# Kernel tuning notes

Hardware: AMD Instinct MI355X
Metric: run time of the kernel (lower is better)

Reference implementation:

```python
import jax, jax.numpy as jnp
import numpy as np

NUM_HEADS = 8
EPS = 1e-6


def conv1x1(x, w, b):
    # x: [b,c,h,w], w: [out,in], b: [out]  (torch Conv2d 1x1 weight squeezed)
    return jnp.einsum('bchw,oc->bohw', x, w) + b[None, :, None, None]


def feature_map(x):
    return jax.nn.elu(x) + 1.0


def setup_inputs() -> dict:
    key = jax.random.key(0)
    ks = jax.random.split(key, 9)
    C = 512
    s = 1.0 / np.sqrt(C)
    x = jax.random.normal(ks[0], (8, C, 64, 64), dtype=jnp.float32)
    wq = jax.random.normal(ks[1], (C, C), dtype=jnp.float32) * s
    wk = jax.random.normal(ks[2], (C, C), dtype=jnp.float32) * s
    wv = jax.random.normal(ks[3], (C, C), dtype=jnp.float32) * s
    wo = jax.random.normal(ks[4], (C, C), dtype=jnp.float32) * s
    bq = jax.random.normal(ks[5], (C,), dtype=jnp.float32) * 0.01
    bk = jax.random.normal(ks[6], (C,), dtype=jnp.float32) * 0.01
    bv = jax.random.normal(ks[7], (C,), dtype=jnp.float32) * 0.01
    bo = jax.random.normal(ks[8], (C,), dtype=jnp.float32) * 0.01
    return {'x': x, 'wq': wq, 'bq': bq, 'wk': wk, 'bk': bk,
            'wv': wv, 'bv': bv, 'wo': wo, 'bo': bo}


def reference(x, wq, bq, wk, bk, wv, bv, wo, bo):
    b, c, h, w = x.shape
    nh = NUM_HEADS
    hd = c // nh
    L = h * w

    def to_heads(t):
        # [b,c,h,w] -> [b,nh,L,hd]
        return t.reshape(b, nh, hd, L).transpose(0, 1, 3, 2)

    Q = feature_map(to_heads(conv1x1(x, wq, bq)))
    K = feature_map(to_heads(conv1x1(x, wk, bk)))
    V = to_heads(conv1x1(x, wv, bv)) / L  # values / v_length

    KV = jnp.einsum('bhld,bhlv->bhdv', K, V)                 # [b,nh,hd,hd]
    Z = 1.0 / (jnp.einsum('bhld,bhd->bhl', Q, K.sum(axis=-2)) + EPS)
    out = jnp.einsum('bhld,bhdv,bhl->bhlv', Q, KV, Z) * L    # [b,nh,L,hd]

    out = out.transpose(0, 1, 3, 2).reshape(b, c, h, w)
    return conv1x1(out, wo, bo)
```

## Files before the change

kernel.cpp:

```cpp
#include <hip/hip_runtime.h>
#include <hip/hip_bf16.h>
#include <stdint.h>

#define BATCH 8
#define CCH   512
#define NHD   8
#define HD    64
#define LLEN  4096
#define M1    1536

typedef __bf16 bf16x8 __attribute__((ext_vector_type(8)));
typedef __bf16 bf16x4 __attribute__((ext_vector_type(4)));
typedef float  f32x4  __attribute__((ext_vector_type(4)));

__device__ __forceinline__ f32x4 mfma16(bf16x8 a, bf16x8 b, f32x4 c) {
  return __builtin_amdgcn_mfma_f32_16x16x32_bf16(a, b, c, 0, 0, 0);
}

__device__ __forceinline__ void gload_lds16(const void* g, void* l) {
  __builtin_amdgcn_global_load_lds(
      (const __attribute__((address_space(1))) uint32_t*)(uintptr_t)g,
      (__attribute__((address_space(3))) uint32_t*)(uintptr_t)l,
      16, 0, 0);
}

__global__ void pack_w(const float* __restrict__ wq, const float* __restrict__ wk,
                       const float* __restrict__ wv, const float* __restrict__ wo,
                       const float* __restrict__ bq, const float* __restrict__ bk,
                       const float* __restrict__ bv,
                       __bf16* __restrict__ wqkvb, __bf16* __restrict__ wob,
                       float* __restrict__ biasq) {
  const int n = M1 * CCH + CCH * CCH + M1;
  for (int i = blockIdx.x * blockDim.x + threadIdx.x; i < n; i += gridDim.x * blockDim.x) {
    if (i < M1 * CCH) {
      int r = i >> 9, c = i & 511;
      float v = (r < 512) ? wq[r * 512 + c]
              : (r < 1024) ? wk[(r - 512) * 512 + c]
                           : wv[(r - 1024) * 512 + c];
      wqkvb[i] = (__bf16)v;
    } else if (i < M1 * CCH + CCH * CCH) {
      int j = i - M1 * CCH;
      wob[j] = (__bf16)wo[j];
    } else {
      int j = i - M1 * CCH - CCH * CCH;
      biasq[j] = (j < 512) ? bq[j] : (j < 1024) ? bk[j - 512] : bv[j - 1024];
    }
  }
}

__global__ __launch_bounds__(256) void transpose_x(const float* __restrict__ x,
                                                   __bf16* __restrict__ xt) {
  __shared__ float tile[64][65];
  const int b = blockIdx.z, c0 = blockIdx.y * 64, l0 = blockIdx.x * 64;
  const int t = threadIdx.x;
  const int lq = (t & 15) * 4, cr = t >> 4;
  const float* xp = x + ((size_t)b * CCH + c0) * LLEN + l0;
#pragma unroll
  for (int q = 0; q < 4; ++q) {
    const int c = cr + q * 16;
    float4 v = *(const float4*)(xp + (size_t)c * LLEN + lq);
    tile[c][lq + 0] = v.x;
    tile[c][lq + 1] = v.y;
    tile[c][lq + 2] = v.z;
    tile[c][lq + 3] = v.w;
  }
  __syncthreads();
  __bf16* xo = xt + ((size_t)b * LLEN + l0) * CCH + c0;
  const int c4 = (t & 15) * 4, lr = t >> 4;
#pragma unroll
  for (int p = 0; p < 4; ++p) {
    const int l = lr + p * 16;
    bf16x4 o;
#pragma unroll
    for (int i = 0; i < 4; ++i) o[i] = (__bf16)tile[c4 + i][l];
    *(bf16x4*)(xo + (size_t)l * CCH + c4) = o;
  }
}

#define STAGE4(tt)                                                           \
  {                                                                          \
    const int tK = (tt) * 32;                                                \
    const int bs = ((tt) % 3) * 16384;                                       \
    gload_lds16(Ag + sOff + tK,         lds + bs + tid * 8);                 \
    gload_lds16(Ag + sOff + 65536 + tK, lds + bs + 4096 + tid * 8);          \
    gload_lds16(Bg + sOff + tK,         lds + bs + 8192 + tid * 8);          \
    gload_lds16(Bg + sOff + 65536 + tK, lds + bs + 12288 + tid * 8);         \
  }
#define READS12(tt)                                                          \
  {                                                                          \
    const int rb = ((tt) % 3) * 16384;                                       \
    const int s = (tt) & 1;                                                  \
    _Pragma("unroll") for (int m = 0; m < 8; ++m)                            \
        aS[s][m] = *(const bf16x8*)(lds + rb + aLane + m * 512);             \
    _Pragma("unroll") for (int n = 0; n < 4; ++n)                            \
        bS[s][n] = *(const bf16x8*)(lds + rb + bLane + n * 512);             \
  }

template <int EPI>
__global__ __launch_bounds__(512, 2) void gemm256(
    const __bf16* __restrict__ A, const __bf16* __restrict__ Bm,
    const float* __restrict__ bias,
    __bf16* __restrict__ qt, __bf16* __restrict__ kcm, __bf16* __restrict__ vcm,
    float* __restrict__ out) {
  __shared__ __attribute__((aligned(16))) __bf16 lds[3 * 16384];
  const int b  = blockIdx.z;
  const int n0 = blockIdx.x * 256;
  const int m0 = blockIdx.y * 256;
  const int tid = threadIdx.x;
  const int ll = tid & 63, w = tid >> 6;
  const int wr = w >> 2, wc = w & 3;
  const int lhi = ll >> 4, llo = ll & 15;

  const int Ra = wr * 128 + llo;
  const int aLane = ((Ra >> 1) << 6) + (((((Ra & 1) << 2) | lhi) ^ ((Ra >> 1) & 7)) << 3);
  const int Rb = wc * 64 + llo;
  const int bLane = 8192 + ((Rb >> 1) << 6) + (((((Rb & 1) << 2) | lhi) ^ ((Rb >> 1) & 7)) << 3);

  const int r2s = tid >> 3, c7u = (tid & 7) ^ (r2s & 7);
  const int sRow = (r2s << 1) | (c7u >> 2);
  const int sOff = sRow * CCH + ((c7u & 3) << 3);

  const __bf16* Ag = A + (size_t)m0 * CCH;
  const __bf16* Bg = Bm + ((size_t)b * LLEN + n0) * CCH;

  bf16x8 aS[2][8], bS[2][4];
  f32x4 acc[8][4] = {};

  STAGE4(0)
  STAGE4(1)
  asm volatile("s_waitcnt vmcnt(4)" ::: "memory");
  asm volatile("s_barrier" ::: "memory");
  READS12(0)

#pragma unroll
  for (int t = 0; t < 16; ++t) {
    asm volatile("s_barrier" ::: "memory");
    if (t < 14) STAGE4(t + 2)
    if (t < 14) asm volatile("s_waitcnt vmcnt(4)" ::: "memory");
    else        asm volatile("s_waitcnt vmcnt(0)" ::: "memory");
    asm volatile("s_barrier" ::: "memory");
    if (t < 15) READS12(t + 1)
    if (t < 15) asm volatile("s_waitcnt lgkmcnt(12)" ::: "memory");
    else        asm volatile("s_waitcnt lgkmcnt(0)" ::: "memory");
    __builtin_amdgcn_sched_barrier(0);
    __builtin_amdgcn_s_setprio(1);
    {
      const int s = t & 1;
#pragma unroll
      for (int m = 0; m < 8; ++m)
#pragma unroll
        for (int n = 0; n < 4; ++n) acc[m][n] = mfma16(aS[s][m], bS[s][n], acc[m][n]);
    }
    __builtin_amdgcn_s_setprio(0);
  }

#pragma unroll
  for (int i = 0; i < 8; ++i) {
    const int o0 = m0 + wr * 128 + i * 16 + lhi * 4;
#pragma unroll
    for (int j = 0; j < 4; ++j) {
      const int col = n0 + wc * 64 + j * 16 + llo;
      if (EPI == 0) {
        if (m0 < 512) {
          bf16x4 pk;
#pragma unroll
          for (int r = 0; r < 4; ++r) {
            float tv = acc[i][j][r] + bias[o0 + r];
            tv = tv > 0.f ? tv + 1.f : __expf(tv);
            pk[r] = (__bf16)tv;
          }
          *(bf16x4*)(qt + ((size_t)b * LLEN + col) * CCH + o0) = pk;
        } else if (m0 < 1024) {
#pragma unroll
          for (int r = 0; r < 4; ++r) {
            float tv = acc[i][j][r] + bias[o0 + r];
            tv = tv > 0.f ? tv + 1.f : __expf(tv);
            kcm[((size_t)b * CCH + (o0 - 512 + r)) * LLEN + col] = (__bf16)tv;
          }
        } else {
#pragma unroll
          for (int r = 0; r < 4; ++r)
            vcm[((size_t)b * CCH + (o0 - 1024 + r)) * LLEN + col] =
                (__bf16)(acc[i][j][r] + bias[o0 + r]);
        }
      } else {
#pragma unroll
        for (int r = 0; r < 4; ++r)
          out[((size_t)b * CCH + o0 + r) * LLEN + col] = acc[i][j][r] + bias[o0 + r];
      }
    }
  }
}

__global__ __launch_bounds__(256) void kv_part_k(const __bf16* __restrict__ kcm,
                                                 const __bf16* __restrict__ vcm,
                                                 float* __restrict__ part,
                                                 float* __restrict__ part_ks) {
  __shared__ float red[8192];
  __shared__ float ksred[4][64];
  const int lc = blockIdx.x, bh = blockIdx.y;
  const int b = bh >> 3, h = bh & 7;
  const int tid = threadIdx.x;
  const int w = tid >> 6, ll = tid & 63, lhi = ll >> 4, llo = ll & 15;
  const __bf16* Kp = kcm + ((size_t)b * CCH + h * 64) * LLEN;
  const __bf16* Vp = vcm + ((size_t)b * CCH + h * 64) * LLEN;
  f32x4 acc[4][4];
#pragma unroll
  for (int i = 0; i < 4; ++i)
#pragma unroll
    for (int j = 0; j < 4; ++j) acc[i][j] = (f32x4){0.f, 0.f, 0.f, 0.f};
  float ks[4] = {0.f, 0.f, 0.f, 0.f};
  const int base = lc * 512 + w * 128 + lhi * 8;
#pragma unroll
  for (int kt = 0; kt < 4; ++kt) {
    const int k0 = base + kt * 32;
    bf16x8 af[4], bfr[4];
#pragma unroll
    for (int i = 0; i < 4; ++i) af[i]  = *(const bf16x8*)(Kp + (size_t)(i * 16 + llo) * LLEN + k0);
#pragma unroll
    for (int i = 0; i < 4; ++i) bfr[i] = *(const bf16x8*)(Vp + (size_t)(i * 16 + llo) * LLEN + k0);
#pragma unroll
    for (int i = 0; i < 4; ++i)
#pragma unroll
      for (int r = 0; r < 8; ++r) ks[i] += (float)af[i][r];
#pragma unroll
    for (int i = 0; i < 4; ++i)
#pragma unroll
      for (int j = 0; j < 4; ++j) acc[i][j] = mfma16(af[i], bfr[j], acc[i][j]);
  }
#pragma unroll
  for (int i = 0; i < 4; ++i) {
    float s = ks[i];
    s += __shfl_xor(s, 16);
    s += __shfl_xor(s, 32);
    if (lhi == 0) ksred[w][i * 16 + llo] = s;
  }
  if (w >= 2) {
#pragma unroll
    for (int i = 0; i < 4; ++i)
#pragma unroll
      for (int j = 0; j < 4; ++j)
        *(f32x4*)(red + (((w - 2) * 16 + i * 4 + j) << 8) + ll * 4) = acc[i][j];
  }
  __syncthreads();
  if (w < 2) {
#pragma unroll
    for (int i = 0; i < 4; ++i)
#pragma unroll
      for (int j = 0; j < 4; ++j)
        acc[i][j] += *(const f32x4*)(red + ((w * 16 + i * 4 + j) << 8) + ll * 4);
  }
  float ksv = 0.f;
  if (w == 1) ksv = ksred[0][ll] + ksred[1][ll] + ksred[2][ll] + ksred[3][ll];
  __syncthreads();
  if (w == 1) {
#pragma unroll
    for (int i = 0; i < 4; ++i)
#pragma unroll
      for (int j = 0; j < 4; ++j)
        *(f32x4*)(red + ((i * 4 + j) << 8) + ll * 4) = acc[i][j];
    part_ks[((size_t)lc * 64 + bh) * 64 + ll] = ksv;
  }
  __syncthreads();
  if (w == 0) {
    float* op = part + ((size_t)lc * 64 + bh) * 4096;
#pragma unroll
    for (int i = 0; i < 4; ++i)
#pragma unroll
      for (int j = 0; j < 4; ++j) {
        acc[i][j] += *(const f32x4*)(red + ((i * 4 + j) << 8) + ll * 4);
#pragma unroll
        for (int r = 0; r < 4; ++r) {
          int d = i * 16 + lhi * 4 + r, v = j * 16 + llo;
          op[d * 64 + v] = acc[i][j][r];
        }
      }
  }
}

__global__ void kv_red_k(const float* __restrict__ part, float* __restrict__ kv) {
  const int i = blockIdx.x * blockDim.x + threadIdx.x;
  float s = 0.f;
#pragma unroll
  for (int lc = 0; lc < 8; ++lc) s += part[(size_t)lc * 262144 + i];
  kv[i] = s;
}

__global__ void ksum_red_k(const float* __restrict__ part_ks, float* __restrict__ ksum) {
  const int i = blockIdx.x * blockDim.x + threadIdx.x;
  float s = 0.f;
#pragma unroll
  for (int lc = 0; lc < 8; ++lc) s += part_ks[(size_t)lc * 4096 + i];
  ksum[i] = s;
}

__global__ __launch_bounds__(256) void apply_k(const __bf16* __restrict__ qt,
                                               const float* __restrict__ kv,
                                               const float* __restrict__ ksum,
                                               __bf16* __restrict__ attn) {
  __shared__ __attribute__((aligned(16))) __bf16 kvT[64 * 68];
  __shared__ float zb[256];
  const int lc = blockIdx.x, bh = blockIdx.y;
  const int b = bh >> 3, h = bh & 7;
  const int tid = threadIdx.x;
  const float* kvp = kv + (size_t)bh * 4096;
  for (int i = tid; i < 4096; i += 256) {
    int d = i >> 6, v = i & 63;
    kvT[v * 68 + d] = (__bf16)kvp[i];
  }
  const int l = lc * 256 + tid;
  const __bf16* qp = qt + ((size_t)b * LLEN + l) * CCH + h * 64;
  const float* ksp = ksum + bh * 64;
  float s = 0.f;
#pragma unroll
  for (int d8 = 0; d8 < 64; d8 += 8) {
    bf16x8 qv = *(const bf16x8*)(qp + d8);
#pragma unroll
    for (int i = 0; i < 8; ++i) s += (float)qv[i] * ksp[d8 + i];
  }
  zb[tid] = 1.0f / (s + 1e-6f);
  __syncthreads();

  const int ll = tid & 63, w = tid >> 6, lhi = ll >> 4, llo = ll & 15;
  f32x4 acc[4][4];
#pragma unroll
  for (int i = 0; i < 4; ++i)
#pragma unroll
    for (int j = 0; j < 4; ++j) acc[i][j] = (f32x4){0.f, 0.f, 0.f, 0.f};
  const __bf16* qbase = qt + ((size_t)b * LLEN + lc * 256 + w * 64) * CCH + h * 64;
#pragma unroll
  for (int kt = 0; kt < 2; ++kt) {
    const int k8 = kt * 32 + lhi * 8;
    bf16x8 af[4], bfr[4];
#pragma unroll
    for (int i = 0; i < 4; ++i)
      af[i] = *(const bf16x8*)(qbase + (size_t)(i * 16 + llo) * CCH + k8);
#pragma unroll
    for (int j = 0; j < 4; ++j) {
      const __bf16* pb = kvT + (j * 16 + llo) * 68 + k8;
      ((bf16x4*)&bfr[j])[0] = *(const bf16x4*)pb;
      ((bf16x4*)&bfr[j])[1] = *(const bf16x4*)(pb + 4);
    }
#pragma unroll
    for (int i = 0; i < 4; ++i)
#pragma unroll
      for (int j = 0; j < 4; ++j) acc[i][j] = mfma16(af[i], bfr[j], acc[i][j]);
  }
  __bf16* ap = attn + ((size_t)b * LLEN + lc * 256) * CCH + h * 64;
#pragma unroll
  for (int i = 0; i < 4; ++i)
#pragma unroll
    for (int j = 0; j < 4; ++j)
#pragma unroll
      for (int r = 0; r < 4; ++r) {
        int ml = w * 64 + i * 16 + lhi * 4 + r;
        int v = j * 16 + llo;
        ap[(size_t)ml * CCH + v] = (__bf16)(acc[i][j][r] * zb[ml]);
      }
}

extern "C" void kernel_launch(void* const* d_in, const int* in_sizes, int n_in,
                              void* d_out, int out_size, void* d_ws, size_t ws_size,
                              hipStream_t stream) {
  const float* x  = (const float*)d_in[0];
  const float* wq = (const float*)d_in[1];
  const float* bq = (const float*)d_in[2];
  const float* wk = (const float*)d_in[3];
  const float* bk = (const float*)d_in[4];
  const float* wv = (const float*)d_in[5];
  const float* bv = (const float*)d_in[6];
  const float* wo = (const float*)d_in[7];
  const float* bo = (const float*)d_in[8];
  float* out = (float*)d_out;

  char* p = (char*)d_ws;
  __bf16* xt    = (__bf16*)p; p += (size_t)BATCH * LLEN * CCH * 2;
  __bf16* qt    = (__bf16*)p; p += (size_t)BATCH * LLEN * CCH * 2;
  __bf16* kcm   = (__bf16*)p; p += (size_t)BATCH * CCH * LLEN * 2;
  __bf16* vcm   = (__bf16*)p; p += (size_t)BATCH * CCH * LLEN * 2;
  __bf16* wqkvb = (__bf16*)p; p += (size_t)M1 * CCH * 2;
  __bf16* wob   = (__bf16*)p; p += (size_t)CCH * CCH * 2;
  float*  biasq = (float*)p;  p += (size_t)M1 * 4;
  float*  ksum  = (float*)p;  p += (size_t)BATCH * CCH * 4;
  float*  part  = (float*)p;  p += (size_t)8 * 64 * HD * HD * 4;
  float*  kvb   = (float*)p;  p += (size_t)64 * HD * HD * 4;
  float*  pks   = (float*)p;  p += (size_t)8 * 64 * 64 * 4;
  __bf16* attn  = xt;

  pack_w<<<1024, 256, 0, stream>>>(wq, wk, wv, wo, bq, bk, bv, wqkvb, wob, biasq);
  transpose_x<<<dim3(64, 8, BATCH), 256, 0, stream>>>(x, xt);
  gemm256<0><<<dim3(16, 6, BATCH), 512, 0, stream>>>(wqkvb, xt, biasq, qt, kcm, vcm, nullptr);
  kv_part_k<<<dim3(8, 64), 256, 0, stream>>>(kcm, vcm, part, pks);
  kv_red_k<<<1024, 256, 0, stream>>>(part, kvb);
  ksum_red_k<<<16, 256, 0, stream>>>(pks, ksum);
  apply_k<<<dim3(16, 64), 256, 0, stream>>>(qt, kvb, ksum, attn);
  gemm256<1><<<dim3(16, 2, BATCH), 512, 0, stream>>>(wob, attn, bo, nullptr, nullptr, nullptr, out);
}
```

Baseline: 170.2 us.

## Restructure GEMM main loop into split-phase ping-pong with 4-stage LDS ring

Replaces the 3-buffer LDS ring and register double-buffered fragments with a 4-buffer ring. Each K step is now split into two half-MFMA phases that interleave LDS fragment reads and the A/B global->LDS prefetch halves, separated by barriers. Launch bounds drop to 1 block per CU to allow the larger LDS footprint and more registers. The intent is to overlap memory and compute the way ping-pong schedules do, at the cost of more barriers per iteration, lower occupancy, and a loop that is no longer forced to unroll.

```diff
diff --git a/kernel.cpp b/kernel.cpp
--- a/kernel.cpp
+++ b/kernel.cpp
@@ -77,32 +77,28 @@
   }
 }
 
-#define STAGE4(tt)                                                           \
+#define STAGE_A2(tt)                                                         \
   {                                                                          \
+    const int bs = ((tt) & 3) * 16384;                                       \
     const int tK = (tt) * 32;                                                \
-    const int bs = ((tt) % 3) * 16384;                                       \
     gload_lds16(Ag + sOff + tK,         lds + bs + tid * 8);                 \
     gload_lds16(Ag + sOff + 65536 + tK, lds + bs + 4096 + tid * 8);          \
+  }
+#define STAGE_B2(tt)                                                         \
+  {                                                                          \
+    const int bs = ((tt) & 3) * 16384;                                       \
+    const int tK = (tt) * 32;                                                \
     gload_lds16(Bg + sOff + tK,         lds + bs + 8192 + tid * 8);          \
     gload_lds16(Bg + sOff + 65536 + tK, lds + bs + 12288 + tid * 8);         \
   }
-#define READS12(tt)                                                          \
-  {                                                                          \
-    const int rb = ((tt) % 3) * 16384;                                       \
-    const int s = (tt) & 1;                                                  \
-    _Pragma("unroll") for (int m = 0; m < 8; ++m)                            \
-        aS[s][m] = *(const bf16x8*)(lds + rb + aLane + m * 512);             \
-    _Pragma("unroll") for (int n = 0; n < 4; ++n)                            \
-        bS[s][n] = *(const bf16x8*)(lds + rb + bLane + n * 512);             \
-  }
 
 template <int EPI>
-__global__ __launch_bounds__(512, 2) void gemm256(
+__global__ __launch_bounds__(512, 1) void gemm256(
     const __bf16* __restrict__ A, const __bf16* __restrict__ Bm,
     const float* __restrict__ bias,
     __bf16* __restrict__ qt, __bf16* __restrict__ kcm, __bf16* __restrict__ vcm,
     float* __restrict__ out) {
-  __shared__ __attribute__((aligned(16))) __bf16 lds[3 * 16384];
+  __shared__ __attribute__((aligned(16))) __bf16 lds[4 * 16384];
   const int b  = blockIdx.z;
   const int n0 = blockIdx.x * 256;
   const int m0 = blockIdx.y * 256;
@@ -123,35 +119,46 @@
   const __bf16* Ag = A + (size_t)m0 * CCH;
   const __bf16* Bg = Bm + ((size_t)b * LLEN + n0) * CCH;
 
-  bf16x8 aS[2][8], bS[2][4];
   f32x4 acc[8][4] = {};
 
-  STAGE4(0)
-  STAGE4(1)
+  STAGE_A2(0) STAGE_B2(0)
+  STAGE_A2(1) STAGE_B2(1)
   asm volatile("s_waitcnt vmcnt(4)" ::: "memory");
   asm volatile("s_barrier" ::: "memory");
-  READS12(0)
-
-#pragma unroll
+
   for (int t = 0; t < 16; ++t) {
+    const int cb = (t & 3) * 16384;
+    bf16x8 af[4], bfr[4];
+#pragma unroll
+    for (int m = 0; m < 4; ++m) af[m] = *(const bf16x8*)(lds + cb + aLane + m * 512);
+#pragma unroll
+    for (int n = 0; n < 4; ++n) bfr[n] = *(const bf16x8*)(lds + cb + bLane + n * 512);
+    if (t <= 13) STAGE_A2(t + 2)
     asm volatile("s_barrier" ::: "memory");
-    if (t < 14) STAGE4(t + 2)
-    if (t < 14) asm volatile("s_waitcnt vmcnt(4)" ::: "memory");
-    else        asm volatile("s_waitcnt vmcnt(0)" ::: "memory");
-    asm volatile("s_barrier" ::: "memory");
-    if (t < 15) READS12(t + 1)
-    if (t < 15) asm volatile("s_waitcnt lgkmcnt(12)" ::: "memory");
-    else        asm volatile("s_waitcnt lgkmcnt(0)" ::: "memory");
+    asm volatile("s_waitcnt lgkmcnt(0)" ::: "memory");
     __builtin_amdgcn_sched_barrier(0);
     __builtin_amdgcn_s_setprio(1);
-    {
-      const int s = t & 1;
-#pragma unroll
-      for (int m = 0; m < 8; ++m)
-#pragma unroll
-        for (int n = 0; n < 4; ++n) acc[m][n] = mfma16(aS[s][m], bS[s][n], acc[m][n]);
-    }
+#pragma unroll
+    for (int m = 0; m < 4; ++m)
+#pragma unroll
+      for (int n = 0; n < 4; ++n) acc[m][n] = mfma16(af[m], bfr[n], acc[m][n]);
     __builtin_amdgcn_s_setprio(0);
+    asm volatile("s_barrier" ::: "memory");
+#pragma unroll
+    for (int m = 0; m < 4; ++m) af[m] = *(const bf16x8*)(lds + cb + aLane + (m + 4) * 512);
+    if (t <= 13) STAGE_B2(t + 2)
+    asm volatile("s_barrier" ::: "memory");
+    asm volatile("s_waitcnt lgkmcnt(0)" ::: "memory");
+    __builtin_amdgcn_sched_barrier(0);
+    __builtin_amdgcn_s_setprio(1);
+#pragma unroll
+    for (int m = 0; m < 4; ++m)
+#pragma unroll
+      for (int n = 0; n < 4; ++n) acc[m + 4][n] = mfma16(af[m], bfr[n], acc[m + 4][n]);
+    __builtin_amdgcn_s_setprio(0);
+    if (t < 14)       asm volatile("s_waitcnt vmcnt(4)" ::: "memory");
+    else if (t == 14) asm volatile("s_waitcnt vmcnt(0)" ::: "memory");
+    asm volatile("s_barrier" ::: "memory");
   }
 
 #pragma unroll
```

New measurement: 176.1 us. +3.4%, slower.

## Pre-tile activations into MFMA fragment layout and use 128x128 GEMM tiles

Applied to the files above, without the earlier changes.

The transpose and apply kernels now write the bf16 activations in a 16-row by 8-column blocked layout that matches the MFMA B-fragment, so the GEMM loads B operands straight from global memory into registers. Only the A (weight) tile goes through a double-buffered LDS. The GEMM shrinks from 256x256 tiles with 512 threads and a triple-buffered LDS pipeline to 128x128 tiles with 256 threads, giving more blocks and higher occupancy. The trade-off is more global traffic for B because it is not shared through LDS, a simpler pipeline with a barrier every k-step, and scattered 2-byte stores in the apply epilogue.

```diff
diff --git a/kernel.cpp b/kernel.cpp
--- a/kernel.cpp
+++ b/kernel.cpp
@@ -23,6 +23,7 @@
       (__attribute__((address_space(3))) uint32_t*)(uintptr_t)l,
       16, 0, 0);
 }
+
 
 __global__ void pack_w(const float* __restrict__ wq, const float* __restrict__ wk,
                        const float* __restrict__ wv, const float* __restrict__ wo,
@@ -65,98 +66,92 @@
     tile[c][lq + 3] = v.w;
   }
   __syncthreads();
-  __bf16* xo = xt + ((size_t)b * LLEN + l0) * CCH + c0;
-  const int c4 = (t & 15) * 4, lr = t >> 4;
-#pragma unroll
-  for (int p = 0; p < 4; ++p) {
-    const int l = lr + p * 16;
-    bf16x4 o;
-#pragma unroll
-    for (int i = 0; i < 4; ++i) o[i] = (__bf16)tile[c4 + i][l];
-    *(bf16x4*)(xo + (size_t)l * CCH + c4) = o;
-  }
-}
-
-#define STAGE4(tt)                                                           \
+  __bf16* xo = xt + (size_t)b * LLEN * CCH;
+  const int c8 = (t & 7) * 8, lr = t >> 3;
+#pragma unroll
+  for (int p = 0; p < 2; ++p) {
+    const int l = lr + p * 32;
+    bf16x8 o;
+#pragma unroll
+    for (int i = 0; i < 8; ++i) o[i] = (__bf16)tile[c8 + i][l];
+    const int gl = l0 + l, gc = c0 + c8;
+    *(bf16x8*)(xo + (gl >> 4) * 8192 + (gc >> 3) * 128 + (gl & 15) * 8) = o;
+  }
+}
+
+#define STG_A(tt, buf)                                                       \
   {                                                                          \
-    const int tK = (tt) * 32;                                                \
-    const int bs = ((tt) % 3) * 16384;                                       \
-    gload_lds16(Ag + sOff + tK,         lds + bs + tid * 8);                 \
-    gload_lds16(Ag + sOff + 65536 + tK, lds + bs + 4096 + tid * 8);          \
-    gload_lds16(Bg + sOff + tK,         lds + bs + 8192 + tid * 8);          \
-    gload_lds16(Bg + sOff + 65536 + tK, lds + bs + 12288 + tid * 8);         \
-  }
-#define READS12(tt)                                                          \
+    const __bf16* As_ = Ag + (tt) * 32;                                      \
+    __bf16* dA = lds + (buf) * 4096;                                         \
+    gload_lds16(As_ + srcOff1, dA + tid * 8);                                \
+    gload_lds16(As_ + srcOff2, dA + tid * 8 + 2048);                         \
+  }
+#define GBODY(t, bqC, bqN)                                                   \
   {                                                                          \
-    const int rb = ((tt) % 3) * 16384;                                       \
-    const int s = (tt) & 1;                                                  \
-    _Pragma("unroll") for (int m = 0; m < 8; ++m)                            \
-        aS[s][m] = *(const bf16x8*)(lds + rb + aLane + m * 512);             \
-    _Pragma("unroll") for (int n = 0; n < 4; ++n)                            \
-        bS[s][n] = *(const bf16x8*)(lds + rb + bLane + n * 512);             \
+    const int buf = (t) & 1;                                                 \
+    if ((t) < 15) {                                                          \
+      STG_A((t) + 1, buf ^ 1)                                                \
+      _Pragma("unroll") for (int n = 0; n < 4; ++n)                          \
+          bqN[n] = *(const bf16x8*)(Bfr[n] + ((t) + 1) * 512);               \
+    }                                                                        \
+    bf16x8 af[4];                                                            \
+    const __bf16* base = lds + buf * 4096;                                   \
+    _Pragma("unroll") for (int m = 0; m < 4; ++m)                            \
+        af[m] = *(const bf16x8*)(base + aOff[m]);                            \
+    _Pragma("unroll") for (int m = 0; m < 4; ++m)                            \
+      _Pragma("unroll") for (int n = 0; n < 4; ++n)                          \
+          acc[m][n] = mfma16(af[m], bqC[n], acc[m][n]);                      \
+    __syncthreads();                                                         \
   }
 
 template <int EPI>
-__global__ __launch_bounds__(512, 2) void gemm256(
+__global__ __launch_bounds__(256, 4) void gemm128(
     const __bf16* __restrict__ A, const __bf16* __restrict__ Bm,
     const float* __restrict__ bias,
     __bf16* __restrict__ qt, __bf16* __restrict__ kcm, __bf16* __restrict__ vcm,
     float* __restrict__ out) {
-  __shared__ __attribute__((aligned(16))) __bf16 lds[3 * 16384];
+  __shared__ __attribute__((aligned(16))) __bf16 lds[2 * 4096];
   const int b  = blockIdx.z;
-  const int n0 = blockIdx.x * 256;
-  const int m0 = blockIdx.y * 256;
+  const int m0 = blockIdx.x * 128;
+  const int n0 = blockIdx.y * 128;
   const int tid = threadIdx.x;
   const int ll = tid & 63, w = tid >> 6;
-  const int wr = w >> 2, wc = w & 3;
+  const int wr = w >> 1, wc = w & 1;
   const int lhi = ll >> 4, llo = ll & 15;
 
-  const int Ra = wr * 128 + llo;
-  const int aLane = ((Ra >> 1) << 6) + (((((Ra & 1) << 2) | lhi) ^ ((Ra >> 1) & 7)) << 3);
-  const int Rb = wc * 64 + llo;
-  const int bLane = 8192 + ((Rb >> 1) << 6) + (((((Rb & 1) << 2) | lhi) ^ ((Rb >> 1) & 7)) << 3);
-
-  const int r2s = tid >> 3, c7u = (tid & 7) ^ (r2s & 7);
-  const int sRow = (r2s << 1) | (c7u >> 2);
-  const int sOff = sRow * CCH + ((c7u & 3) << 3);
+  const int slotE = ((lhi ^ ((llo >> 1) & 3)) << 3);
+  int aOff[4];
+#pragma unroll
+  for (int m = 0; m < 4; ++m) aOff[m] = (wr * 64 + m * 16 + llo) * 32 + slotE;
+
+  const int s1 = tid, s2 = tid + 256;
+  const int r1 = s1 >> 2, r2 = s2 >> 2;
+  const int srcOff1 = r1 * CCH + (((s1 & 3) ^ ((r1 >> 1) & 3)) << 3);
+  const int srcOff2 = r2 * CCH + (((s2 & 3) ^ ((r2 >> 1) & 3)) << 3);
 
   const __bf16* Ag = A + (size_t)m0 * CCH;
-  const __bf16* Bg = Bm + ((size_t)b * LLEN + n0) * CCH;
-
-  bf16x8 aS[2][8], bS[2][4];
-  f32x4 acc[8][4] = {};
-
-  STAGE4(0)
-  STAGE4(1)
-  asm volatile("s_waitcnt vmcnt(4)" ::: "memory");
-  asm volatile("s_barrier" ::: "memory");
-  READS12(0)
-
-#pragma unroll
-  for (int t = 0; t < 16; ++t) {
-    asm volatile("s_barrier" ::: "memory");
-    if (t < 14) STAGE4(t + 2)
-    if (t < 14) asm volatile("s_waitcnt vmcnt(4)" ::: "memory");
-    else        asm volatile("s_waitcnt vmcnt(0)" ::: "memory");
-    asm volatile("s_barrier" ::: "memory");
-    if (t < 15) READS12(t + 1)
-    if (t < 15) asm volatile("s_waitcnt lgkmcnt(12)" ::: "memory");
-    else        asm volatile("s_waitcnt lgkmcnt(0)" ::: "memory");
-    __builtin_amdgcn_sched_barrier(0);
-    __builtin_amdgcn_s_setprio(1);
-    {
-      const int s = t & 1;
-#pragma unroll
-      for (int m = 0; m < 8; ++m)
-#pragma unroll
-        for (int n = 0; n < 4; ++n) acc[m][n] = mfma16(aS[s][m], bS[s][n], acc[m][n]);
-    }
-    __builtin_amdgcn_s_setprio(0);
-  }
-
-#pragma unroll
-  for (int i = 0; i < 8; ++i) {
-    const int o0 = m0 + wr * 128 + i * 16 + lhi * 4;
+  const __bf16* Bt = Bm + (size_t)b * LLEN * CCH;
+  const __bf16* Bfr[4];
+#pragma unroll
+  for (int n = 0; n < 4; ++n)
+    Bfr[n] = Bt + ((n0 + wc * 64 + n * 16) >> 4) * 8192 + llo * 8 + lhi * 128;
+
+  f32x4 acc[4][4] = {};
+  bf16x8 bqA[4], bqB[4];
+
+#pragma unroll
+  for (int n = 0; n < 4; ++n) bqA[n] = *(const bf16x8*)(Bfr[n]);
+  STG_A(0, 0)
+  __syncthreads();
+
+  for (int tt = 0; tt < 8; ++tt) {
+    GBODY(2 * tt, bqA, bqB)
+    GBODY(2 * tt + 1, bqB, bqA)
+  }
+
+#pragma unroll
+  for (int i = 0; i < 4; ++i) {
+    const int o0 = m0 + wr * 64 + i * 16 + lhi * 4;
 #pragma unroll
     for (int j = 0; j < 4; ++j) {
       const int col = n0 + wc * 64 + j * 16 + llo;
@@ -346,16 +341,17 @@
 #pragma unroll
       for (int j = 0; j < 4; ++j) acc[i][j] = mfma16(af[i], bfr[j], acc[i][j]);
   }
-  __bf16* ap = attn + ((size_t)b * LLEN + lc * 256) * CCH + h * 64;
+  __bf16* ap = attn + (size_t)b * LLEN * CCH;
 #pragma unroll
   for (int i = 0; i < 4; ++i)
 #pragma unroll
     for (int j = 0; j < 4; ++j)
 #pragma unroll
       for (int r = 0; r < 4; ++r) {
-        int ml = w * 64 + i * 16 + lhi * 4 + r;
-        int v = j * 16 + llo;
-        ap[(size_t)ml * CCH + v] = (__bf16)(acc[i][j][r] * zb[ml]);
+        int gl = lc * 256 + w * 64 + i * 16 + lhi * 4 + r;
+        int gc = h * 64 + j * 16 + llo;
+        ap[(gl >> 4) * 8192 + (gc >> 3) * 128 + (gl & 15) * 8 + (gc & 7)] =
+            (__bf16)(acc[i][j][r] * zb[w * 64 + i * 16 + lhi * 4 + r]);
       }
 }
 
@@ -389,10 +385,11 @@
 
   pack_w<<<1024, 256, 0, stream>>>(wq, wk, wv, wo, bq, bk, bv, wqkvb, wob, biasq);
   transpose_x<<<dim3(64, 8, BATCH), 256, 0, stream>>>(x, xt);
-  gemm256<0><<<dim3(16, 6, BATCH), 512, 0, stream>>>(wqkvb, xt, biasq, qt, kcm, vcm, nullptr);
+  gemm128<0><<<dim3(12, 32, BATCH), 256, 0, stream>>>(wqkvb, xt, biasq, qt, kcm, vcm, nullptr);
   kv_part_k<<<dim3(8, 64), 256, 0, stream>>>(kcm, vcm, part, pks);
   kv_red_k<<<1024, 256, 0, stream>>>(part, kvb);
   ksum_red_k<<<16, 256, 0, stream>>>(pks, ksum);
   apply_k<<<dim3(16, 64), 256, 0, stream>>>(qt, kvb, ksum, attn);
-  gemm256<1><<<dim3(16, 2, BATCH), 512, 0, stream>>>(wob, attn, bo, nullptr, nullptr, nullptr, out);
-}
+  gemm128<1><<<dim3(4, 32, BATCH), 256, 0, stream>>>(wob, attn, bo, nullptr, nullptr,
+                                                     nullptr, out);
+}
```

Measured after the change: 186.4 us. +9.5%, slower.
